# Optimization experiments

Hardware: AMD Instinct MI355X
Metric: run time of the kernel (lower is better)

The kernel has to match this reference:

```python
import jax, jax.numpy as jnp
import numpy as np

HEADS = 8
HEAD_DIM = 64
SCALE = HEAD_DIM ** -0.5


def setup_inputs() -> dict:
    key = jax.random.key(0)
    k1, k2, k3 = jax.random.split(key, 3)
    b, p, n, dim = 8, 16, 256, 384
    inner = HEADS * HEAD_DIM  # 512
    x = jax.random.normal(k1, (b, p, n, dim), dtype=jnp.float32)
    w_qkv = jax.random.normal(k2, (dim, 3 * inner), dtype=jnp.float32) * (dim ** -0.5)
    w_out = jax.random.normal(k3, (inner, dim), dtype=jnp.float32) * (inner ** -0.5)
    b_out = jnp.zeros((dim,), dtype=jnp.float32)
    return {"x": x, "w_qkv": w_qkv, "w_out": w_out, "b_out": b_out}


def reference(x, w_qkv, w_out, b_out):
    b, p, n, dim = x.shape
    inner = HEADS * HEAD_DIM
    qkv = jnp.einsum('bpnd,de->bpne', x, w_qkv)  # [b,p,n,3*inner]
    q, k, v = jnp.split(qkv, 3, axis=-1)
    # [b,p,n,inner] -> [b,p,h,n,hd]
    def to_heads(t):
        return t.reshape(b, p, n, HEADS, HEAD_DIM).transpose(0, 1, 3, 2, 4)
    q, k, v = to_heads(q), to_heads(k), to_heads(v)
    dots = jnp.einsum('bphqd,bphkd->bphqk', q, k) * SCALE
    attn = jax.nn.softmax(dots, axis=-1)
    out = jnp.einsum('bphqk,bphkd->bphqd', attn, v)
    out = out.transpose(0, 1, 3, 2, 4).reshape(b, p, n, inner)
    return jnp.einsum('bpni,id->bpnd', out, w_out) + b_out
```

## Files before the change

kernel.cpp:

```cpp
#include <hip/hip_runtime.h>
#include <stdint.h>

#define DEVFN __device__ __forceinline__

typedef __attribute__((ext_vector_type(8))) __bf16 bf16x8;
typedef __attribute__((ext_vector_type(8))) short short8;
typedef __attribute__((ext_vector_type(4))) float f32x4;
typedef __attribute__((ext_vector_type(4))) unsigned int u32x4;

DEVFN unsigned short f2bf(float f) {
  return __builtin_bit_cast(unsigned short, (__bf16)f);
}

DEVFN void gload_lds16(const void* g, void* l) {
  __builtin_amdgcn_global_load_lds(
      (const __attribute__((address_space(1))) void*)(uintptr_t)g,
      (__attribute__((address_space(3))) void*)(uint32_t)(uintptr_t)l,
      16, 0, 0);
}


__global__ void k_prep(const float* __restrict__ wqkv, const float* __restrict__ wout,
                       short* __restrict__ Wqt, short* __restrict__ Wot) {
  int i = blockIdx.x * blockDim.x + threadIdx.x;
  if (i < 589824) {
    int c = i / 384, r = i - c * 384;
    Wqt[i] = (short)f2bf(wqkv[(size_t)r * 1536 + c]);
  } else {
    int j = i - 589824;
    if (j < 196608) {
      int c = j / 512, r = j - c * 512;
      Wot[j] = (short)f2bf(wout[(size_t)r * 384 + c]);
    }
  }
}


#define LOADA(A0, A1, A2, A3, T)                                             \
  do {                                                                       \
    const float* bA = X + (size_t)(m0 + rowA) * 384 + (T) * 32 + slA * 8;    \
    A0 = *(const f32x4*)bA;                                                  \
    A1 = *(const f32x4*)(bA + 4);                                            \
    A2 = *(const f32x4*)(bA + 64 * 384);                                     \
    A3 = *(const f32x4*)(bA + 64 * 384 + 4);                                 \
  } while (0)

#define WRITEA(BUF, A0, A1, A2, A3)                                          \
  do {                                                                       \
    u32x4 w0_;                                                               \
    w0_[0] = (unsigned)f2bf(A0[0]) | ((unsigned)f2bf(A0[1]) << 16);          \
    w0_[1] = (unsigned)f2bf(A0[2]) | ((unsigned)f2bf(A0[3]) << 16);          \
    w0_[2] = (unsigned)f2bf(A1[0]) | ((unsigned)f2bf(A1[1]) << 16);          \
    w0_[3] = (unsigned)f2bf(A1[2]) | ((unsigned)f2bf(A1[3]) << 16);          \
    *(u32x4*)&As[BUF][tid * 8] = w0_;                                        \
    u32x4 w1_;                                                               \
    w1_[0] = (unsigned)f2bf(A2[0]) | ((unsigned)f2bf(A2[1]) << 16);          \
    w1_[1] = (unsigned)f2bf(A2[2]) | ((unsigned)f2bf(A2[3]) << 16);          \
    w1_[2] = (unsigned)f2bf(A3[0]) | ((unsigned)f2bf(A3[1]) << 16);          \
    w1_[3] = (unsigned)f2bf(A3[2]) | ((unsigned)f2bf(A3[3]) << 16);          \
    *(u32x4*)&As[BUF][(tid + 256) * 8] = w1_;                                \
  } while (0)

#define STEP_MAIN(T, C0, C1, C2, C3, N0, N1, N2, N3)                         \
  do {                                                                       \
    asm volatile("s_waitcnt vmcnt(4) lgkmcnt(0)" ::: "memory");              \
    __builtin_amdgcn_sched_barrier(0);                                       \
    __builtin_amdgcn_s_barrier();                                            \
    __builtin_amdgcn_sched_barrier(0);                                       \
    LOADA(N0, N1, N2, N3, (T) + 2);                                          \
    stageB(((T) + 2) % 3, (T) + 2);                                          \
    WRITEA(((T) + 1) % 3, C0, C1, C2, C3);                                   \
    compute((T) % 3);                                                        \
  } while (0)

__global__ __launch_bounds__(256, 2)
void k_gemm1(const float* __restrict__ X, const short* __restrict__ Bt,
             unsigned short* __restrict__ Cb) {
  __shared__ short As[3][128 * 32];
  __shared__ short Bs[3][256 * 32];
  const int tid = threadIdx.x, l = tid & 63, w = tid >> 6;
  const int nwg = gridDim.x, cpx = nwg >> 3;
  const int bid = (blockIdx.x & 7) * cpx + (blockIdx.x >> 3);
  const int mt = bid / 6, nt = bid % 6;
  const int m0 = mt << 7, n0 = nt * 256;
  const int wm = (w >> 1) << 6, wn = (w & 1) * 128;
  const int rowA = tid >> 2;
  const int slA = (tid & 3) ^ ((rowA >> 1) & 3);

  f32x4 acc[4][8];
#pragma unroll
  for (int i = 0; i < 4; i++)
#pragma unroll
    for (int j = 0; j < 8; j++) acc[i][j] = (f32x4){0.f, 0.f, 0.f, 0.f};

  auto stageB = [&](int buf, int t) {
#pragma unroll
    for (int c = 0; c < 4; ++c) {
      int ch = tid + c * 256;
      int row = ch >> 2;
      int sl = (ch & 3) ^ ((row >> 1) & 3);
      gload_lds16(Bt + (size_t)(n0 + row) * 384 + t * 32 + sl * 8, &Bs[buf][ch * 8]);
    }
  };
  const int sp8 = (((l >> 4) ^ ((l >> 1) & 3)) << 3);
  auto compute = [&](int buf) {
    bf16x8 af[4], bfr[8];
#pragma unroll
    for (int i = 0; i < 4; i++)
      af[i] = *(const bf16x8*)&As[buf][(wm + i * 16 + (l & 15)) * 32 + sp8];
#pragma unroll
    for (int j = 0; j < 8; j++)
      bfr[j] = *(const bf16x8*)&Bs[buf][(wn + j * 16 + (l & 15)) * 32 + sp8];
#pragma unroll
    for (int i = 0; i < 4; i++)
#pragma unroll
      for (int j = 0; j < 8; j++)
        acc[i][j] = __builtin_amdgcn_mfma_f32_16x16x32_bf16(af[i], bfr[j], acc[i][j], 0, 0, 0);
  };

  f32x4 a0_, a1_, a2_, a3_, b0_, b1_, b2_, b3_;
  LOADA(a0_, a1_, a2_, a3_, 0);
  LOADA(b0_, b1_, b2_, b3_, 1);
  stageB(0, 0);
  stageB(1, 1);
  asm volatile("s_waitcnt vmcnt(12)" ::: "memory");
  WRITEA(0, a0_, a1_, a2_, a3_);

#pragma unroll 1
  for (int tp = 0; tp < 10; tp += 2) {
    STEP_MAIN(tp,     b0_, b1_, b2_, b3_, a0_, a1_, a2_, a3_);
    STEP_MAIN(tp + 1, a0_, a1_, a2_, a3_, b0_, b1_, b2_, b3_);
  }
  asm volatile("s_waitcnt vmcnt(4) lgkmcnt(0)" ::: "memory");
  __builtin_amdgcn_sched_barrier(0);
  __builtin_amdgcn_s_barrier();
  __builtin_amdgcn_sched_barrier(0);
  WRITEA(2, b0_, b1_, b2_, b3_);
  compute(1);
  asm volatile("s_waitcnt vmcnt(0) lgkmcnt(0)" ::: "memory");
  __builtin_amdgcn_sched_barrier(0);
  __builtin_amdgcn_s_barrier();
  __builtin_amdgcn_sched_barrier(0);
  compute(2);

#pragma unroll
  for (int i = 0; i < 4; i++) {
    int mrow = m0 + wm + i * 16 + ((l >> 4) << 2);
#pragma unroll
    for (int j = 0; j < 8; j++) {
      int ncol = n0 + wn + j * 16 + (l & 15);
#pragma unroll
      for (int r = 0; r < 4; r++)
        Cb[(size_t)(mrow + r) * 1536 + ncol] = f2bf(acc[i][j][r]);
    }
  }
}


__global__ __launch_bounds__(512, 2)
void k_gemm2(const short* __restrict__ A, const short* __restrict__ Bt,
             float* __restrict__ Cf, const float* __restrict__ bias) {
  __shared__ short As[3][256 * 32];
  __shared__ short Bs[3][128 * 32];
  const int tid = threadIdx.x;
  const int l = tid & 63, w = tid >> 6;
  const int nwg = gridDim.x, cpx = nwg >> 3;
  const int bid = (blockIdx.x & 7) * cpx + (blockIdx.x >> 3);
  const int mt = bid / 3, nt = bid % 3;
  const int m0 = mt << 8, n0 = nt << 7;
  const int wm = (w >> 1) << 6, wn = (w & 1) << 6;

  f32x4 acc[4][4];
#pragma unroll
  for (int i = 0; i < 4; i++)
#pragma unroll
    for (int j = 0; j < 4; j++) acc[i][j] = (f32x4){0.f, 0.f, 0.f, 0.f};

  const int nsteps = 16;

  auto stage = [&](int buf, int t) {
#pragma unroll
    for (int c = 0; c < 2; ++c) {
      int ch = tid + c * 512;
      int row = ch >> 2;
      int sl = (ch & 3) ^ ((row >> 1) & 3);
      gload_lds16(A + (size_t)(m0 + row) * 512 + t * 32 + sl * 8, &As[buf][ch * 8]);
    }
    {
      int ch = tid;
      int row = ch >> 2;
      int sl = (ch & 3) ^ ((row >> 1) & 3);
      gload_lds16(Bt + (size_t)(n0 + row) * 512 + t * 32 + sl * 8, &Bs[buf][ch * 8]);
    }
  };
  const int sp8 = (((l >> 4) ^ ((l >> 1) & 3)) << 3);
  auto compute = [&](int buf) {
    bf16x8 af[4], bfr[4];
#pragma unroll
    for (int i = 0; i < 4; i++)
      af[i] = *(const bf16x8*)&As[buf][(wm + i * 16 + (l & 15)) * 32 + sp8];
#pragma unroll
    for (int j = 0; j < 4; j++)
      bfr[j] = *(const bf16x8*)&Bs[buf][(wn + j * 16 + (l & 15)) * 32 + sp8];
#pragma unroll
    for (int i = 0; i < 4; i++)
#pragma unroll
      for (int j = 0; j < 4; j++)
        acc[i][j] = __builtin_amdgcn_mfma_f32_16x16x32_bf16(af[i], bfr[j], acc[i][j], 0, 0, 0);
  };

  stage(0, 0);
  stage(1, 1);
#pragma unroll 1
  for (int t = 0; t < nsteps; ++t) {
    if (t + 1 < nsteps) {
      asm volatile("s_waitcnt vmcnt(3)" ::: "memory");
    } else {
      asm volatile("s_waitcnt vmcnt(0)" ::: "memory");
    }
    __builtin_amdgcn_sched_barrier(0);
    __builtin_amdgcn_s_barrier();
    __builtin_amdgcn_sched_barrier(0);
    if (t + 2 < nsteps) stage((t + 2) % 3, t + 2);
    compute(t % 3);
  }

#pragma unroll
  for (int i = 0; i < 4; i++) {
    int mrow = m0 + wm + i * 16 + ((l >> 4) << 2);
#pragma unroll
    for (int j = 0; j < 4; j++) {
      int ncol = n0 + wn + j * 16 + (l & 15);
#pragma unroll
      for (int r = 0; r < 4; r++)
        Cf[(size_t)(mrow + r) * 384 + ncol] = acc[i][j][r] + bias[ncol];
    }
  }
}


__global__ __launch_bounds__(512, 2)
void k_attn(const short* __restrict__ qkv, unsigned short* __restrict__ O) {
  __shared__ short Kl[256 * 64];
  __shared__ short Vt[64 * 256];

  const int tid = threadIdx.x, l = tid & 63, w = tid >> 6;
  const int g = (l >> 4) & 3;
  const int bh = blockIdx.x;
  const int bp = bh >> 3, h = bh & 7;
  const size_t tokbase = (size_t)bp * 256 * 1536;
  const int qoff = h * 64, koff = 512 + h * 64, voff = 1024 + h * 64;

#pragma unroll
  for (int c = 0; c < 4; ++c) {
    int ch = tid + c * 512;
    int row = ch >> 3, s = ch & 7;
    int sg = s ^ (row & 7);
    gload_lds16(qkv + tokbase + (size_t)row * 1536 + koff + sg * 8, &Kl[ch * 8]);
  }
#pragma unroll
  for (int c = 0; c < 4; ++c) {
    int ch = tid + c * 512;
    int row = ch >> 3, d0 = (ch & 7) * 8;
    short8 v = *(const short8*)(qkv + tokbase + (size_t)row * 1536 + voff + d0);
    int kc = row >> 5, u = row & 31;
    int gg = (u >> 2) & 3;
    int off = ((u & 16) ? 4 : 0) + (u & 3);
#pragma unroll
    for (int j = 0; j < 8; ++j) {
      int d = d0 + j;
      int sl = (kc * 4 + gg) ^ (d & 15);
      Vt[d * 256 + sl * 8 + off] = v[j];
    }
  }
  __syncthreads();

  const float CEXP = 0.125f * 1.44269504f;

#pragma unroll 1
  for (int it = 0; it < 2; ++it) {
    const int q0 = w * 32 + it * 16;
    bf16x8 qa[2];
#pragma unroll
    for (int dc = 0; dc < 2; ++dc)
      qa[dc] = *(const bf16x8*)(qkv + tokbase + (size_t)(q0 + (l & 15)) * 1536 + qoff +
                                dc * 32 + (l >> 4) * 8);
    f32x4 s[16];
#pragma unroll
    for (int kt = 0; kt < 16; kt++) s[kt] = (f32x4){0.f, 0.f, 0.f, 0.f};
    __builtin_amdgcn_s_setprio(1);
#pragma unroll
    for (int dc = 0; dc < 2; ++dc) {
#pragma unroll
      for (int kt = 0; kt < 16; ++kt) {
        int kcol = kt * 16 + (l & 15);
        int sl = (dc * 4 + (l >> 4)) ^ (kcol & 7);
        bf16x8 kb = *(const bf16x8*)&Kl[kcol * 64 + sl * 8];
        s[kt] = __builtin_amdgcn_mfma_f32_16x16x32_bf16(kb, qa[dc], s[kt], 0, 0, 0);
      }
    }
    __builtin_amdgcn_s_setprio(0);
    float mx = s[0][0];
#pragma unroll
    for (int kt = 0; kt < 16; kt++)
#pragma unroll
      for (int r = 0; r < 4; r++) mx = fmaxf(mx, s[kt][r]);
    mx = fmaxf(mx, __shfl_xor(mx, 16, 64));
    mx = fmaxf(mx, __shfl_xor(mx, 32, 64));

    u32x4 pa[8];
    float sum = 0.f;
#pragma unroll
    for (int kc = 0; kc < 8; ++kc) {
      float p0 = exp2f((s[2 * kc][0] - mx) * CEXP);
      float p1 = exp2f((s[2 * kc][1] - mx) * CEXP);
      float p2 = exp2f((s[2 * kc][2] - mx) * CEXP);
      float p3 = exp2f((s[2 * kc][3] - mx) * CEXP);
      float p4 = exp2f((s[2 * kc + 1][0] - mx) * CEXP);
      float p5 = exp2f((s[2 * kc + 1][1] - mx) * CEXP);
      float p6 = exp2f((s[2 * kc + 1][2] - mx) * CEXP);
      float p7 = exp2f((s[2 * kc + 1][3] - mx) * CEXP);
      sum += ((p0 + p1) + (p2 + p3)) + ((p4 + p5) + (p6 + p7));
      u32x4 pw;
      pw[0] = (unsigned)f2bf(p0) | ((unsigned)f2bf(p1) << 16);
      pw[1] = (unsigned)f2bf(p2) | ((unsigned)f2bf(p3) << 16);
      pw[2] = (unsigned)f2bf(p4) | ((unsigned)f2bf(p5) << 16);
      pw[3] = (unsigned)f2bf(p6) | ((unsigned)f2bf(p7) << 16);
      pa[kc] = pw;
    }
    sum += __shfl_xor(sum, 16, 64);
    sum += __shfl_xor(sum, 32, 64);
    float rs = 1.0f / sum;

    f32x4 o[4];
#pragma unroll
    for (int dt = 0; dt < 4; dt++) o[dt] = (f32x4){0.f, 0.f, 0.f, 0.f};
#pragma unroll
    for (int kc = 0; kc < 8; ++kc) {
      bf16x8 paf = __builtin_bit_cast(bf16x8, pa[kc]);
      __builtin_amdgcn_s_setprio(1);
#pragma unroll
      for (int dt = 0; dt < 4; ++dt) {
        int d = dt * 16 + (l & 15);
        int sl = (kc * 4 + g) ^ (d & 15);
        bf16x8 vb = *(const bf16x8*)&Vt[d * 256 + sl * 8];
        o[dt] = __builtin_amdgcn_mfma_f32_16x16x32_bf16(paf, vb, o[dt], 0, 0, 0);
      }
      __builtin_amdgcn_s_setprio(0);
      __builtin_amdgcn_sched_barrier(0);
    }
    float rsq[4];
#pragma unroll
    for (int r = 0; r < 4; ++r)
      rsq[r] = __shfl(rs, (l & 48) | (g * 4 + r), 64);
#pragma unroll
    for (int dt = 0; dt < 4; dt++) {
#pragma unroll
      for (int r = 0; r < 4; r++) {
        int qrow = q0 + g * 4 + r;
        int d = dt * 16 + (l & 15);
        O[(size_t)(bp * 256 + qrow) * 512 + h * 64 + d] = f2bf(o[dt][r] * rsq[r]);
      }
    }
  }
}


extern "C" void kernel_launch(void* const* d_in, const int* in_sizes, int n_in,
                              void* d_out, int out_size, void* d_ws, size_t ws_size,
                              hipStream_t stream) {
  const float* x    = (const float*)d_in[0];
  const float* wqkv = (const float*)d_in[1];
  const float* wout = (const float*)d_in[2];
  const float* bout = (const float*)d_in[3];
  float* out = (float*)d_out;
  char* ws = (char*)d_ws;

  short* Wot = (short*)(ws);
  short* Wqt = (short*)(ws + 25559040);
  unsigned short* O = (unsigned short*)(ws + 393216);
  short* QKV = (short*)(ws + 33947648);

  k_prep<<<3072, 256, 0, stream>>>(wqkv, wout, Wqt, Wot);
  k_gemm1<<<1536, 256, 0, stream>>>(x, Wqt, (unsigned short*)QKV);
  k_attn<<<1024, 512, 0, stream>>>(QKV, O);
  k_gemm2<<<384, 512, 0, stream>>>((const short*)O, Wot, out, bout);
  (void)in_sizes; (void)n_in; (void)out_size; (void)ws_size;
}
```

Before: 124.8 us.

## Double k_gemm1 threads to 512 with 4x2 wave grid and 64x64 warp tiles

Raises the QKV projection GEMM from 256 to 512 threads per block, so each of the 8 waves computes a 64x64 sub-tile instead of 64x128. Each thread now loads and converts half as much A and B data per K step, and the vmcnt waits are adjusted to match. The aim is more waves available to hide latency and fewer accumulator registers per thread. In exchange, the LDS fragment reads per MFMA rise because each wave reuses its A fragments across fewer B columns.

```diff
diff --git a/kernel.cpp b/kernel.cpp
--- a/kernel.cpp
+++ b/kernel.cpp
@@ -36,16 +36,14 @@
 }
 
 
-#define LOADA(A0, A1, A2, A3, T)                                             \
+#define LOADA(A0, A1, T)                                                     \
   do {                                                                       \
     const float* bA = X + (size_t)(m0 + rowA) * 384 + (T) * 32 + slA * 8;    \
     A0 = *(const f32x4*)bA;                                                  \
     A1 = *(const f32x4*)(bA + 4);                                            \
-    A2 = *(const f32x4*)(bA + 64 * 384);                                     \
-    A3 = *(const f32x4*)(bA + 64 * 384 + 4);                                 \
   } while (0)
 
-#define WRITEA(BUF, A0, A1, A2, A3)                                          \
+#define WRITEA(BUF, A0, A1)                                                  \
   do {                                                                       \
     u32x4 w0_;                                                               \
     w0_[0] = (unsigned)f2bf(A0[0]) | ((unsigned)f2bf(A0[1]) << 16);          \
@@ -53,27 +51,21 @@
     w0_[2] = (unsigned)f2bf(A1[0]) | ((unsigned)f2bf(A1[1]) << 16);          \
     w0_[3] = (unsigned)f2bf(A1[2]) | ((unsigned)f2bf(A1[3]) << 16);          \
     *(u32x4*)&As[BUF][tid * 8] = w0_;                                        \
-    u32x4 w1_;                                                               \
-    w1_[0] = (unsigned)f2bf(A2[0]) | ((unsigned)f2bf(A2[1]) << 16);          \
-    w1_[1] = (unsigned)f2bf(A2[2]) | ((unsigned)f2bf(A2[3]) << 16);          \
-    w1_[2] = (unsigned)f2bf(A3[0]) | ((unsigned)f2bf(A3[1]) << 16);          \
-    w1_[3] = (unsigned)f2bf(A3[2]) | ((unsigned)f2bf(A3[3]) << 16);          \
-    *(u32x4*)&As[BUF][(tid + 256) * 8] = w1_;                                \
   } while (0)
 
-#define STEP_MAIN(T, C0, C1, C2, C3, N0, N1, N2, N3)                         \
+#define STEP_MAIN(T, C0, C1, N0, N1)                                         \
   do {                                                                       \
-    asm volatile("s_waitcnt vmcnt(4) lgkmcnt(0)" ::: "memory");              \
+    asm volatile("s_waitcnt vmcnt(2) lgkmcnt(0)" ::: "memory");              \
     __builtin_amdgcn_sched_barrier(0);                                       \
     __builtin_amdgcn_s_barrier();                                            \
     __builtin_amdgcn_sched_barrier(0);                                       \
-    LOADA(N0, N1, N2, N3, (T) + 2);                                          \
+    LOADA(N0, N1, (T) + 2);                                                  \
     stageB(((T) + 2) % 3, (T) + 2);                                          \
-    WRITEA(((T) + 1) % 3, C0, C1, C2, C3);                                   \
+    WRITEA(((T) + 1) % 3, C0, C1);                                           \
     compute((T) % 3);                                                        \
   } while (0)
 
-__global__ __launch_bounds__(256, 2)
+__global__ __launch_bounds__(512, 2)
 void k_gemm1(const float* __restrict__ X, const short* __restrict__ Bt,
              unsigned short* __restrict__ Cb) {
   __shared__ short As[3][128 * 32];
@@ -83,20 +75,20 @@
   const int bid = (blockIdx.x & 7) * cpx + (blockIdx.x >> 3);
   const int mt = bid / 6, nt = bid % 6;
   const int m0 = mt << 7, n0 = nt * 256;
-  const int wm = (w >> 1) << 6, wn = (w & 1) * 128;
+  const int wm = (w >> 2) << 6, wn = (w & 3) << 6;
   const int rowA = tid >> 2;
   const int slA = (tid & 3) ^ ((rowA >> 1) & 3);
 
-  f32x4 acc[4][8];
+  f32x4 acc[4][4];
 #pragma unroll
   for (int i = 0; i < 4; i++)
 #pragma unroll
-    for (int j = 0; j < 8; j++) acc[i][j] = (f32x4){0.f, 0.f, 0.f, 0.f};
+    for (int j = 0; j < 4; j++) acc[i][j] = (f32x4){0.f, 0.f, 0.f, 0.f};
 
   auto stageB = [&](int buf, int t) {
 #pragma unroll
-    for (int c = 0; c < 4; ++c) {
-      int ch = tid + c * 256;
+    for (int c = 0; c < 2; ++c) {
+      int ch = tid + c * 512;
       int row = ch >> 2;
       int sl = (ch & 3) ^ ((row >> 1) & 3);
       gload_lds16(Bt + (size_t)(n0 + row) * 384 + t * 32 + sl * 8, &Bs[buf][ch * 8]);
@@ -104,38 +96,38 @@
   };
   const int sp8 = (((l >> 4) ^ ((l >> 1) & 3)) << 3);
   auto compute = [&](int buf) {
-    bf16x8 af[4], bfr[8];
+    bf16x8 af[4], bfr[4];
 #pragma unroll
     for (int i = 0; i < 4; i++)
       af[i] = *(const bf16x8*)&As[buf][(wm + i * 16 + (l & 15)) * 32 + sp8];
 #pragma unroll
-    for (int j = 0; j < 8; j++)
+    for (int j = 0; j < 4; j++)
       bfr[j] = *(const bf16x8*)&Bs[buf][(wn + j * 16 + (l & 15)) * 32 + sp8];
 #pragma unroll
     for (int i = 0; i < 4; i++)
 #pragma unroll
-      for (int j = 0; j < 8; j++)
+      for (int j = 0; j < 4; j++)
         acc[i][j] = __builtin_amdgcn_mfma_f32_16x16x32_bf16(af[i], bfr[j], acc[i][j], 0, 0, 0);
   };
 
-  f32x4 a0_, a1_, a2_, a3_, b0_, b1_, b2_, b3_;
-  LOADA(a0_, a1_, a2_, a3_, 0);
-  LOADA(b0_, b1_, b2_, b3_, 1);
+  f32x4 a0_, a1_, b0_, b1_;
+  LOADA(a0_, a1_, 0);
+  LOADA(b0_, b1_, 1);
   stageB(0, 0);
   stageB(1, 1);
-  asm volatile("s_waitcnt vmcnt(12)" ::: "memory");
-  WRITEA(0, a0_, a1_, a2_, a3_);
+  asm volatile("s_waitcnt vmcnt(6)" ::: "memory");
+  WRITEA(0, a0_, a1_);
 
 #pragma unroll 1
   for (int tp = 0; tp < 10; tp += 2) {
-    STEP_MAIN(tp,     b0_, b1_, b2_, b3_, a0_, a1_, a2_, a3_);
-    STEP_MAIN(tp + 1, a0_, a1_, a2_, a3_, b0_, b1_, b2_, b3_);
-  }
-  asm volatile("s_waitcnt vmcnt(4) lgkmcnt(0)" ::: "memory");
+    STEP_MAIN(tp,     b0_, b1_, a0_, a1_);
+    STEP_MAIN(tp + 1, a0_, a1_, b0_, b1_);
+  }
+  asm volatile("s_waitcnt vmcnt(2) lgkmcnt(0)" ::: "memory");
   __builtin_amdgcn_sched_barrier(0);
   __builtin_amdgcn_s_barrier();
   __builtin_amdgcn_sched_barrier(0);
-  WRITEA(2, b0_, b1_, b2_, b3_);
+  WRITEA(2, b0_, b1_);
   compute(1);
   asm volatile("s_waitcnt vmcnt(0) lgkmcnt(0)" ::: "memory");
   __builtin_amdgcn_sched_barrier(0);
@@ -147,7 +139,7 @@
   for (int i = 0; i < 4; i++) {
     int mrow = m0 + wm + i * 16 + ((l >> 4) << 2);
 #pragma unroll
-    for (int j = 0; j < 8; j++) {
+    for (int j = 0; j < 4; j++) {
       int ncol = n0 + wn + j * 16 + (l & 15);
 #pragma unroll
       for (int r = 0; r < 4; r++)
@@ -382,7 +374,7 @@
   short* QKV = (short*)(ws + 33947648);
 
   k_prep<<<3072, 256, 0, stream>>>(wqkv, wout, Wqt, Wot);
-  k_gemm1<<<1536, 256, 0, stream>>>(x, Wqt, (unsigned short*)QKV);
+  k_gemm1<<<1536, 512, 0, stream>>>(x, Wqt, (unsigned short*)QKV);
   k_attn<<<1024, 512, 0, stream>>>(QKV, O);
   k_gemm2<<<384, 512, 0, stream>>>((const short*)O, Wot, out, bout);
   (void)in_sizes; (void)n_in; (void)out_size; (void)ws_size;
```

Measured after the change: 122.1 us. -2.2%, faster.
